# Performance work log

Measured on AMD Instinct MI355X. Metric: run time of the kernel, lower is better.

Reference implementation:

```python
import jax, jax.numpy as jnp
import numpy as np
from jax import lax

T = 64
TAU = 2.0
ALPHA = 4.0  # spikingjelly surrogate.Sigmoid default
V_TH = 1.0

@jax.custom_vjp
def spike(v):
    # Heaviside(v) with sigmoid surrogate gradient
    return (v >= 0.0).astype(v.dtype)

def _spike_fwd(v):
    return spike(v), v

def _spike_bwd(v, g):
    s = jax.nn.sigmoid(ALPHA * v)
    return (g * ALPHA * s * (1.0 - s),)

spike.defvjp(_spike_fwd, _spike_bwd)

def setup_inputs() -> dict:
    key = jax.random.key(0)
    k1, k2, k3 = jax.random.split(key, 3)
    x = jax.random.normal(k1, (2048, 28, 28), dtype=jnp.float32)
    W1 = jax.random.normal(k2, (1024, 784), dtype=jnp.float32) * (1.0 / np.sqrt(784))
    W2 = jax.random.normal(k3, (10, 1024), dtype=jnp.float32) * (1.0 / np.sqrt(1024))
    return {"x": x, "W1": W1, "W2": W2}

def _lif_step(v, c):
    # decay_input=True: v += (x - (v - v_reset)) / tau, v_reset = 0
    v = v + (c - v) / TAU
    s = spike(v - V_TH)
    v = v * (1.0 - s)  # hard reset to 0
    return v, s

def reference(x, W1, W2):
    B = x.shape[0]
    xf = x.reshape(B, -1)                      # [B, 784]
    c1 = xf @ W1.T                              # [B, 1024], identical every timestep
    v1_0 = jnp.zeros((B, W1.shape[0]), x.dtype)
    v2_0 = jnp.zeros((B, W2.shape[0]), x.dtype)

    def step(carry, _):
        v1, v2 = carry
        v1, s1 = _lif_step(v1, c1)              # [B, 1024]
        c2 = s1 @ W2.T                          # [B, 10]
        v2, s2 = _lif_step(v2, c2)              # [B, 10]
        return (v1, v2), s2

    _, out = lax.scan(step, (v1_0, v2_0), None, length=T)
    return out  # [T, B, 10]
```

## Files before the change

### kernel.cpp

```cpp
#include <hip/hip_runtime.h>
#include <stdint.h>

typedef unsigned long long u64;
typedef unsigned int u32;

#define T_STEPS 64
#define KDIM 784
#define N1 1024
#define NB 2048
#define N2 10

__global__ void k_w2t(const float* __restrict__ W2, float* __restrict__ W2T) {
    int j = blockIdx.x * blockDim.x + threadIdx.x;
    if (j >= N1) return;
    float r[12];
#pragma unroll
    for (int i = 0; i < 10; ++i) r[i] = W2[i * N1 + j];
    r[10] = 0.f; r[11] = 0.f;
#pragma unroll
    for (int i = 0; i < 12; ++i) W2T[j * 12 + i] = r[i];
}

__global__ __launch_bounds__(256) void k_transpose2(
    const float* __restrict__ X, float* __restrict__ Xt,
    const float* __restrict__ W1, float* __restrict__ W1t)
{
    __shared__ float t[32][33];
    int b = blockIdx.x;
    const float* src; float* dst; int R;
    int tile_r, tile_c;
    if (b < 1600) { src = X;  dst = Xt;  R = NB; tile_r = b / 25; tile_c = b % 25; }
    else { b -= 1600; src = W1; dst = W1t; R = N1; tile_r = b / 25; tile_c = b % 25; }

    const int tx = threadIdx.x & 31, ty = threadIdx.x >> 5;
    const int r0 = tile_r << 5, c0 = tile_c << 5;

#pragma unroll
    for (int i = 0; i < 32; i += 8) {
        int c = c0 + tx;
        t[ty + i][tx] = (c < KDIM) ? src[(size_t)(r0 + ty + i) * KDIM + c] : 0.f;
    }
    __syncthreads();
#pragma unroll
    for (int i = 0; i < 32; i += 8) {
        int c = c0 + ty + i;
        if (c < KDIM) dst[(size_t)c * R + r0 + tx] = t[tx][ty + i];
    }
}

#define NSTEP (KDIM / 16)

typedef const __attribute__((address_space(1))) void gas_void;
typedef __attribute__((address_space(3))) void las_void;

__global__ __launch_bounds__(256) void k_gemm_lif1(
    const float* __restrict__ Xt,
    const float* __restrict__ W1t,
    u64* __restrict__ bits)
{
    __shared__ __align__(16) float A2[4][16][64];
    __shared__ __align__(16) float B2[4][16][64];

    const int tid  = threadIdx.x;
    const int lane = tid & 63;
    const int tx   = tid & 15;
    const int ty   = tid >> 4;
    const int bm   = blockIdx.y << 6;
    const int bn   = blockIdx.x << 6;

    const int w4   = __builtin_amdgcn_readfirstlane((tid >> 6) << 2);
    const int srow = w4 + (lane >> 4);
    const int scol = (lane & 15) << 2;

    const float* gA = Xt  + (size_t)srow * NB + bm + scol;
    const float* gB = W1t + (size_t)srow * N1 + bn + scol;

#define STAGE(pp, t)                                                          \
    {                                                                         \
        __builtin_amdgcn_global_load_lds((gas_void*)(gA + (size_t)(t) * (16 * NB)), \
                                         (las_void*)&A2[pp][w4][0], 16, 0, 0); \
        __builtin_amdgcn_global_load_lds((gas_void*)(gB + (size_t)(t) * (16 * N1)), \
                                         (las_void*)&B2[pp][w4][0], 16, 0, 0); \
    }

#define COMPUTE(cur)                                                          \
    _Pragma("unroll")                                                         \
    for (int kk = 0; kk < 16; ++kk) {                                         \
        float4 av = *(const float4*)(&A2[cur][kk][ty << 2]);                  \
        float4 bv = *(const float4*)(&B2[cur][kk][tx << 2]);                  \
        acc[0][0] = fmaf(av.x, bv.x, acc[0][0]); acc[0][1] = fmaf(av.x, bv.y, acc[0][1]); \
        acc[0][2] = fmaf(av.x, bv.z, acc[0][2]); acc[0][3] = fmaf(av.x, bv.w, acc[0][3]); \
        acc[1][0] = fmaf(av.y, bv.x, acc[1][0]); acc[1][1] = fmaf(av.y, bv.y, acc[1][1]); \
        acc[1][2] = fmaf(av.y, bv.z, acc[1][2]); acc[1][3] = fmaf(av.y, bv.w, acc[1][3]); \
        acc[2][0] = fmaf(av.z, bv.x, acc[2][0]); acc[2][1] = fmaf(av.z, bv.y, acc[2][1]); \
        acc[2][2] = fmaf(av.z, bv.z, acc[2][2]); acc[2][3] = fmaf(av.z, bv.w, acc[2][3]); \
        acc[3][0] = fmaf(av.w, bv.x, acc[3][0]); acc[3][1] = fmaf(av.w, bv.y, acc[3][1]); \
        acc[3][2] = fmaf(av.w, bv.z, acc[3][2]); acc[3][3] = fmaf(av.w, bv.w, acc[3][3]); \
    }

    float acc[4][4];
#pragma unroll
    for (int r = 0; r < 4; ++r)
#pragma unroll
        for (int c = 0; c < 4; ++c) acc[r][c] = 0.f;

    STAGE(0, 0);
    STAGE(1, 1);

    for (int t = 0; t < NSTEP - 1; ++t) {
        asm volatile("s_waitcnt vmcnt(2)" ::: "memory");
        __builtin_amdgcn_sched_barrier(0);
        __builtin_amdgcn_s_barrier();
        __builtin_amdgcn_sched_barrier(0);
        if (t + 2 < NSTEP) STAGE((t + 2) & 3, t + 2);
        __builtin_amdgcn_sched_barrier(0);
        const int cur = t & 3;
        COMPUTE(cur);
        __builtin_amdgcn_sched_barrier(0);
    }
    asm volatile("s_waitcnt vmcnt(0)" ::: "memory");
    __builtin_amdgcn_sched_barrier(0);
    __builtin_amdgcn_s_barrier();
    __builtin_amdgcn_sched_barrier(0);
    {
        const int cur = (NSTEP - 1) & 3;
        COMPUTE(cur);
    }
#undef STAGE
#undef COMPUTE

    float c[16], v[16];
    u32 blo[16], bhi[16];
#pragma unroll
    for (int u = 0; u < 16; ++u) {
        c[u] = acc[u >> 2][u & 3];
        v[u] = 0.f; blo[u] = 0u; bhi[u] = 0u;
    }
    for (int t = 0; t < 32; ++t) {
#pragma unroll
        for (int u = 0; u < 16; ++u) {
            v[u] += (c[u] - v[u]) * 0.5f;
            bool s = v[u] >= 1.0f;
            blo[u] |= (s ? 1u : 0u) << t;
            v[u] = s ? 0.f : v[u];
        }
    }
    for (int t = 0; t < 32; ++t) {
#pragma unroll
        for (int u = 0; u < 16; ++u) {
            v[u] += (c[u] - v[u]) * 0.5f;
            bool s = v[u] >= 1.0f;
            bhi[u] |= (s ? 1u : 0u) << t;
            v[u] = s ? 0.f : v[u];
        }
    }
#pragma unroll
    for (int u = 0; u < 16; ++u) {
        int r = u >> 2, cc = u & 3;
        bits[(size_t)(bm + (ty << 2) + r) * N1 + (bn + (tx << 2) + cc)] =
            ((u64)bhi[u] << 32) | (u64)blo[u];
    }
}

__global__ __launch_bounds__(256) void k_c2(
    const u64* __restrict__ bits, const float* __restrict__ W2T,
    float* __restrict__ c2d)
{
    __shared__ u64  masksS[N1];
    __shared__ u32  idxS[N1];
    __shared__ float c2S[4][64][12];

    const int tid  = threadIdx.x;
    const int w    = tid >> 6;
    const int lane = tid & 63;
    const int b    = blockIdx.x;

    const u64* row = bits + (size_t)b * N1;
    const int base_j = w << 8;

    u64 mm[4];
#pragma unroll
    for (int q = 0; q < 4; ++q) mm[q] = row[base_j + (q << 6) + lane];

    int nact = 0;
#pragma unroll
    for (int q = 0; q < 4; ++q) {
        u64 ball = __ballot(mm[q] != 0ULL);
        int pos = nact + __popcll(ball & ((1ULL << lane) - 1ULL));
        if (mm[q] != 0ULL) { masksS[base_j + pos] = mm[q]; idxS[base_j + pos] = base_j + (q << 6) + lane; }
        nact += __popcll(ball);
    }
    const int npad = (nact + 3) & ~3;
    if (lane < npad - nact) { masksS[base_j + nact + lane] = 0ULL; idxS[base_j + nact + lane] = 0u; }

    float acc[10];
#pragma unroll
    for (int i = 0; i < 10; ++i) acc[i] = 0.f;

    for (int a = 0; a < npad; a += 4) {
        u64 m[4]; u32 j[4];
#pragma unroll
        for (int q = 0; q < 4; ++q) {
            m[q] = masksS[base_j + a + q];
            j[q] = idxS[base_j + a + q];
        }
#pragma unroll
        for (int q = 0; q < 4; ++q) {
            float sf = (float)((m[q] >> lane) & 1ULL);
            const float* wr = W2T + j[q] * 12;
            float4 w0 = *(const float4*)(wr);
            float4 w1 = *(const float4*)(wr + 4);
            float2 w2 = *(const float2*)(wr + 8);
            acc[0] = fmaf(sf, w0.x, acc[0]); acc[1] = fmaf(sf, w0.y, acc[1]);
            acc[2] = fmaf(sf, w0.z, acc[2]); acc[3] = fmaf(sf, w0.w, acc[3]);
            acc[4] = fmaf(sf, w1.x, acc[4]); acc[5] = fmaf(sf, w1.y, acc[5]);
            acc[6] = fmaf(sf, w1.z, acc[6]); acc[7] = fmaf(sf, w1.w, acc[7]);
            acc[8] = fmaf(sf, w2.x, acc[8]); acc[9] = fmaf(sf, w2.y, acc[9]);
        }
    }

#pragma unroll
    for (int i = 0; i < 10; ++i) c2S[w][lane][i] = acc[i];
    __syncthreads();

    for (int idx = tid; idx < 64 * 10; idx += 256) {
        int t = idx / 10, i = idx % 10;
        c2d[(size_t)b * 640 + idx] = ((c2S[0][t][i] + c2S[1][t][i]) + c2S[2][t][i]) + c2S[3][t][i];
    }
}

__global__ __launch_bounds__(256) void k_out(
    const float* __restrict__ c2d, float* __restrict__ out)
{
    const int p = blockIdx.x * 256 + threadIdx.x;
    const int b = p / 10, i = p % 10;
    const float* src = c2d + (size_t)b * 640 + i;

    float v2 = 0.f;
    for (int tb = 0; tb < 64; tb += 8) {
        float cc[8];
#pragma unroll
        for (int q = 0; q < 8; ++q) cc[q] = src[(tb + q) * 10];
#pragma unroll
        for (int q = 0; q < 8; ++q) {
            v2 += (cc[q] - v2) * 0.5f;
            bool s = v2 >= 1.0f;
            out[(size_t)(tb + q) * (NB * N2) + p] = s ? 1.f : 0.f;
            v2 = s ? 0.f : v2;
        }
    }
}

extern "C" void kernel_launch(void* const* d_in, const int* in_sizes, int n_in,
                              void* d_out, int out_size, void* d_ws, size_t ws_size,
                              hipStream_t stream) {
    const float* X  = (const float*)d_in[0];
    const float* W1 = (const float*)d_in[1];
    const float* W2 = (const float*)d_in[2];
    float* out = (float*)d_out;

    char* ws = (char*)d_ws;
    u64*   bits = (u64*)ws;
    float* W2T  = (float*)(ws + (size_t)NB * N1 * 8);
    float* Xt   = (float*)(ws + (size_t)NB * N1 * 8 + 65536);
    float* W1t  = Xt + (size_t)KDIM * NB;
    float* c2d  = W1t + (size_t)KDIM * N1;

    k_w2t<<<dim3((N1 + 255) / 256), dim3(256), 0, stream>>>(W2, W2T);
    k_transpose2<<<dim3(2400), dim3(256), 0, stream>>>(X, Xt, W1, W1t);

    dim3 g1(N1 / 64, NB / 64);
    k_gemm_lif1<<<g1, dim3(256), 0, stream>>>(Xt, W1t, bits);

    k_c2<<<dim3(NB), dim3(256), 0, stream>>>(bits, W2T, c2d);
    k_out<<<dim3(20480 / 256), dim3(256), 0, stream>>>(c2d, out);
}
```

Before: 180.1 us.

## Fuse prep kernels, register-prefetch GEMM, and fold output LIF into c2 kernel

```diff
diff --git a/kernel.cpp b/kernel.cpp
--- a/kernel.cpp
+++ b/kernel.cpp
@@ -10,23 +10,25 @@
 #define NB 2048
 #define N2 10
 
-__global__ void k_w2t(const float* __restrict__ W2, float* __restrict__ W2T) {
-    int j = blockIdx.x * blockDim.x + threadIdx.x;
-    if (j >= N1) return;
-    float r[12];
-#pragma unroll
-    for (int i = 0; i < 10; ++i) r[i] = W2[i * N1 + j];
-    r[10] = 0.f; r[11] = 0.f;
-#pragma unroll
-    for (int i = 0; i < 12; ++i) W2T[j * 12 + i] = r[i];
-}
-
-__global__ __launch_bounds__(256) void k_transpose2(
+__global__ __launch_bounds__(256) void k_prep(
     const float* __restrict__ X, float* __restrict__ Xt,
-    const float* __restrict__ W1, float* __restrict__ W1t)
+    const float* __restrict__ W1, float* __restrict__ W1t,
+    const float* __restrict__ W2, float* __restrict__ W2T)
 {
+    int b = blockIdx.x;
+    if (b == 2400) {
+        for (int it = 0; it < 4; ++it) {
+            int j = it * 256 + threadIdx.x;
+            float r[12];
+#pragma unroll
+            for (int i = 0; i < 10; ++i) r[i] = W2[i * N1 + j];
+            r[10] = 0.f; r[11] = 0.f;
+#pragma unroll
+            for (int i = 0; i < 12; ++i) W2T[j * 12 + i] = r[i];
+        }
+        return;
+    }
     __shared__ float t[32][33];
-    int b = blockIdx.x;
     const float* src; float* dst; int R;
     int tile_r, tile_c;
     if (b < 1600) { src = X;  dst = Xt;  R = NB; tile_r = b / 25; tile_c = b % 25; }
@@ -48,55 +50,28 @@
     }
 }
 
-#define NSTEP (KDIM / 16)
-
-typedef const __attribute__((address_space(1))) void gas_void;
-typedef __attribute__((address_space(3))) void las_void;
-
-__global__ __launch_bounds__(256) void k_gemm_lif1(
+__global__ __launch_bounds__(256, 2) void k_gemm_lif1(
     const float* __restrict__ Xt,
     const float* __restrict__ W1t,
     u64* __restrict__ bits)
 {
-    __shared__ __align__(16) float A2[4][16][64];
-    __shared__ __align__(16) float B2[4][16][64];
-
-    const int tid  = threadIdx.x;
-    const int lane = tid & 63;
-    const int tx   = tid & 15;
-    const int ty   = tid >> 4;
-    const int bm   = blockIdx.y << 6;
-    const int bn   = blockIdx.x << 6;
-
-    const int w4   = __builtin_amdgcn_readfirstlane((tid >> 6) << 2);
-    const int srow = w4 + (lane >> 4);
-    const int scol = (lane & 15) << 2;
-
-    const float* gA = Xt  + (size_t)srow * NB + bm + scol;
-    const float* gB = W1t + (size_t)srow * N1 + bn + scol;
-
-#define STAGE(pp, t)                                                          \
-    {                                                                         \
-        __builtin_amdgcn_global_load_lds((gas_void*)(gA + (size_t)(t) * (16 * NB)), \
-                                         (las_void*)&A2[pp][w4][0], 16, 0, 0); \
-        __builtin_amdgcn_global_load_lds((gas_void*)(gB + (size_t)(t) * (16 * N1)), \
-                                         (las_void*)&B2[pp][w4][0], 16, 0, 0); \
-    }
-
-#define COMPUTE(cur)                                                          \
-    _Pragma("unroll")                                                         \
-    for (int kk = 0; kk < 16; ++kk) {                                         \
-        float4 av = *(const float4*)(&A2[cur][kk][ty << 2]);                  \
-        float4 bv = *(const float4*)(&B2[cur][kk][tx << 2]);                  \
-        acc[0][0] = fmaf(av.x, bv.x, acc[0][0]); acc[0][1] = fmaf(av.x, bv.y, acc[0][1]); \
-        acc[0][2] = fmaf(av.x, bv.z, acc[0][2]); acc[0][3] = fmaf(av.x, bv.w, acc[0][3]); \
-        acc[1][0] = fmaf(av.y, bv.x, acc[1][0]); acc[1][1] = fmaf(av.y, bv.y, acc[1][1]); \
-        acc[1][2] = fmaf(av.y, bv.z, acc[1][2]); acc[1][3] = fmaf(av.y, bv.w, acc[1][3]); \
-        acc[2][0] = fmaf(av.z, bv.x, acc[2][0]); acc[2][1] = fmaf(av.z, bv.y, acc[2][1]); \
-        acc[2][2] = fmaf(av.z, bv.z, acc[2][2]); acc[2][3] = fmaf(av.z, bv.w, acc[2][3]); \
-        acc[3][0] = fmaf(av.w, bv.x, acc[3][0]); acc[3][1] = fmaf(av.w, bv.y, acc[3][1]); \
-        acc[3][2] = fmaf(av.w, bv.z, acc[3][2]); acc[3][3] = fmaf(av.w, bv.w, acc[3][3]); \
-    }
+    const int tid = threadIdx.x;
+    const int tx  = tid & 15;
+    const int ty  = tid >> 4;
+    const int bm  = blockIdx.y << 6;
+    const int bn  = blockIdx.x << 6;
+
+#define LOAD_A(k) (*(const float4*)(Xt  + (size_t)(k) * NB + bm + (ty << 2)))
+#define LOAD_B(k) (*(const float4*)(W1t + (size_t)(k) * N1 + bn + (tx << 2)))
+#define FMAS(av, bv)                                                                      \
+    acc[0][0] = fmaf(av.x, bv.x, acc[0][0]); acc[0][1] = fmaf(av.x, bv.y, acc[0][1]);     \
+    acc[0][2] = fmaf(av.x, bv.z, acc[0][2]); acc[0][3] = fmaf(av.x, bv.w, acc[0][3]);     \
+    acc[1][0] = fmaf(av.y, bv.x, acc[1][0]); acc[1][1] = fmaf(av.y, bv.y, acc[1][1]);     \
+    acc[1][2] = fmaf(av.y, bv.z, acc[1][2]); acc[1][3] = fmaf(av.y, bv.w, acc[1][3]);     \
+    acc[2][0] = fmaf(av.z, bv.x, acc[2][0]); acc[2][1] = fmaf(av.z, bv.y, acc[2][1]);     \
+    acc[2][2] = fmaf(av.z, bv.z, acc[2][2]); acc[2][3] = fmaf(av.z, bv.w, acc[2][3]);     \
+    acc[3][0] = fmaf(av.w, bv.x, acc[3][0]); acc[3][1] = fmaf(av.w, bv.y, acc[3][1]);     \
+    acc[3][2] = fmaf(av.w, bv.z, acc[3][2]); acc[3][3] = fmaf(av.w, bv.w, acc[3][3]);
 
     float acc[4][4];
 #pragma unroll
@@ -104,30 +79,27 @@
 #pragma unroll
         for (int c = 0; c < 4; ++c) acc[r][c] = 0.f;
 
-    STAGE(0, 0);
-    STAGE(1, 1);
-
-    for (int t = 0; t < NSTEP - 1; ++t) {
-        asm volatile("s_waitcnt vmcnt(2)" ::: "memory");
-        __builtin_amdgcn_sched_barrier(0);
-        __builtin_amdgcn_s_barrier();
-        __builtin_amdgcn_sched_barrier(0);
-        if (t + 2 < NSTEP) STAGE((t + 2) & 3, t + 2);
-        __builtin_amdgcn_sched_barrier(0);
-        const int cur = t & 3;
-        COMPUTE(cur);
-        __builtin_amdgcn_sched_barrier(0);
-    }
-    asm volatile("s_waitcnt vmcnt(0)" ::: "memory");
-    __builtin_amdgcn_sched_barrier(0);
-    __builtin_amdgcn_s_barrier();
-    __builtin_amdgcn_sched_barrier(0);
-    {
-        const int cur = (NSTEP - 1) & 3;
-        COMPUTE(cur);
-    }
-#undef STAGE
-#undef COMPUTE
+    float4 pa[16], pb[16];
+#pragma unroll
+    for (int q = 0; q < 16; ++q) { pa[q] = LOAD_A(q); pb[q] = LOAD_B(q); }
+
+    for (int t = 0; t < 48; ++t) {
+#pragma unroll
+        for (int q = 0; q < 16; ++q) {
+            float4 av = pa[q], bv = pb[q];
+            pa[q] = LOAD_A(t * 16 + 16 + q);
+            pb[q] = LOAD_B(t * 16 + 16 + q);
+            FMAS(av, bv);
+        }
+    }
+#pragma unroll
+    for (int q = 0; q < 16; ++q) {
+        float4 av = pa[q], bv = pb[q];
+        FMAS(av, bv);
+    }
+#undef LOAD_A
+#undef LOAD_B
+#undef FMAS
 
     float c[16], v[16];
     u32 blo[16], bhi[16];
@@ -162,13 +134,16 @@
     }
 }
 
-__global__ __launch_bounds__(256) void k_c2(
+__global__ __launch_bounds__(256) void k_c2lif(
     const u64* __restrict__ bits, const float* __restrict__ W2T,
-    float* __restrict__ c2d)
+    float* __restrict__ out)
 {
-    __shared__ u64  masksS[N1];
-    __shared__ u32  idxS[N1];
+    __shared__ u64   masksS[N1];
+    __shared__ u32   idxS[N1];
+    __shared__ float wS[4][64][12];
     __shared__ float c2S[4][64][12];
+    __shared__ float c2r[64][12];
+    __shared__ float s2S[64][10];
 
     const int tid  = threadIdx.x;
     const int w    = tid >> 6;
@@ -192,30 +167,42 @@
     }
     const int npad = (nact + 3) & ~3;
     if (lane < npad - nact) { masksS[base_j + nact + lane] = 0ULL; idxS[base_j + nact + lane] = 0u; }
+    asm volatile("s_waitcnt lgkmcnt(0)" ::: "memory");
 
     float acc[10];
 #pragma unroll
     for (int i = 0; i < 10; ++i) acc[i] = 0.f;
 
-    for (int a = 0; a < npad; a += 4) {
-        u64 m[4]; u32 j[4];
-#pragma unroll
-        for (int q = 0; q < 4; ++q) {
-            m[q] = masksS[base_j + a + q];
-            j[q] = idxS[base_j + a + q];
-        }
-#pragma unroll
-        for (int q = 0; q < 4; ++q) {
-            float sf = (float)((m[q] >> lane) & 1ULL);
-            const float* wr = W2T + j[q] * 12;
-            float4 w0 = *(const float4*)(wr);
-            float4 w1 = *(const float4*)(wr + 4);
-            float2 w2 = *(const float2*)(wr + 8);
-            acc[0] = fmaf(sf, w0.x, acc[0]); acc[1] = fmaf(sf, w0.y, acc[1]);
-            acc[2] = fmaf(sf, w0.z, acc[2]); acc[3] = fmaf(sf, w0.w, acc[3]);
-            acc[4] = fmaf(sf, w1.x, acc[4]); acc[5] = fmaf(sf, w1.y, acc[5]);
-            acc[6] = fmaf(sf, w1.z, acc[6]); acc[7] = fmaf(sf, w1.w, acc[7]);
-            acc[8] = fmaf(sf, w2.x, acc[8]); acc[9] = fmaf(sf, w2.y, acc[9]);
+    for (int base = 0; base < npad; base += 64) {
+        const int cnt = min(64, npad - base);
+        if (lane < cnt) {
+            int j = (int)idxS[base_j + base + lane];
+            const float4* src = (const float4*)(W2T + j * 12);
+            float4 a = src[0], bq = src[1], cq = src[2];
+            *(float4*)&wS[w][lane][0] = a;
+            *(float4*)&wS[w][lane][4] = bq;
+            *(float4*)&wS[w][lane][8] = cq;
+        }
+        asm volatile("s_waitcnt lgkmcnt(0) vmcnt(0)" ::: "memory");
+        __builtin_amdgcn_sched_barrier(0);
+
+        for (int a = 0; a < cnt; a += 4) {
+            u64 m[4];
+#pragma unroll
+            for (int q = 0; q < 4; ++q) m[q] = masksS[base_j + base + a + q];
+#pragma unroll
+            for (int q = 0; q < 4; ++q) {
+                float sf = (float)((m[q] >> lane) & 1ULL);
+                const float* wr = &wS[w][a + q][0];
+                float4 w0 = *(const float4*)(wr);
+                float4 w1 = *(const float4*)(wr + 4);
+                float2 w2 = *(const float2*)(wr + 8);
+                acc[0] = fmaf(sf, w0.x, acc[0]); acc[1] = fmaf(sf, w0.y, acc[1]);
+                acc[2] = fmaf(sf, w0.z, acc[2]); acc[3] = fmaf(sf, w0.w, acc[3]);
+                acc[4] = fmaf(sf, w1.x, acc[4]); acc[5] = fmaf(sf, w1.y, acc[5]);
+                acc[6] = fmaf(sf, w1.z, acc[6]); acc[7] = fmaf(sf, w1.w, acc[7]);
+                acc[8] = fmaf(sf, w2.x, acc[8]); acc[9] = fmaf(sf, w2.y, acc[9]);
+            }
         }
     }
 
@@ -225,29 +212,31 @@
 
     for (int idx = tid; idx < 64 * 10; idx += 256) {
         int t = idx / 10, i = idx % 10;
-        c2d[(size_t)b * 640 + idx] = ((c2S[0][t][i] + c2S[1][t][i]) + c2S[2][t][i]) + c2S[3][t][i];
-    }
-}
-
-__global__ __launch_bounds__(256) void k_out(
-    const float* __restrict__ c2d, float* __restrict__ out)
-{
-    const int p = blockIdx.x * 256 + threadIdx.x;
-    const int b = p / 10, i = p % 10;
-    const float* src = c2d + (size_t)b * 640 + i;
-
-    float v2 = 0.f;
-    for (int tb = 0; tb < 64; tb += 8) {
-        float cc[8];
-#pragma unroll
-        for (int q = 0; q < 8; ++q) cc[q] = src[(tb + q) * 10];
-#pragma unroll
-        for (int q = 0; q < 8; ++q) {
-            v2 += (cc[q] - v2) * 0.5f;
-            bool s = v2 >= 1.0f;
-            out[(size_t)(tb + q) * (NB * N2) + p] = s ? 1.f : 0.f;
-            v2 = s ? 0.f : v2;
-        }
+        c2r[t][i] = ((c2S[0][t][i] + c2S[1][t][i]) + c2S[2][t][i]) + c2S[3][t][i];
+    }
+    __syncthreads();
+
+    if (tid < 10) {
+        const int i = tid;
+        float v2 = 0.f;
+        for (int tb = 0; tb < 64; tb += 8) {
+            float cc[8];
+#pragma unroll
+            for (int q = 0; q < 8; ++q) cc[q] = c2r[tb + q][i];
+#pragma unroll
+            for (int q = 0; q < 8; ++q) {
+                v2 += (cc[q] - v2) * 0.5f;
+                bool s = v2 >= 1.0f;
+                s2S[tb + q][i] = s ? 1.f : 0.f;
+                v2 = s ? 0.f : v2;
+            }
+        }
+    }
+    __syncthreads();
+
+    for (int idx = tid; idx < 64 * 10; idx += 256) {
+        int t = idx / 10, i = idx % 10;
+        out[(size_t)t * (NB * N2) + (size_t)b * N2 + i] = s2S[t][i];
     }
 }
 
@@ -264,14 +253,11 @@
     float* W2T  = (float*)(ws + (size_t)NB * N1 * 8);
     float* Xt   = (float*)(ws + (size_t)NB * N1 * 8 + 65536);
     float* W1t  = Xt + (size_t)KDIM * NB;
-    float* c2d  = W1t + (size_t)KDIM * N1;
-
-    k_w2t<<<dim3((N1 + 255) / 256), dim3(256), 0, stream>>>(W2, W2T);
-    k_transpose2<<<dim3(2400), dim3(256), 0, stream>>>(X, Xt, W1, W1t);
+
+    k_prep<<<dim3(2401), dim3(256), 0, stream>>>(X, Xt, W1, W1t, W2, W2T);
 
     dim3 g1(N1 / 64, NB / 64);
     k_gemm_lif1<<<g1, dim3(256), 0, stream>>>(Xt, W1t, bits);
 
-    k_c2<<<dim3(NB), dim3(256), 0, stream>>>(bits, W2T, c2d);
-    k_out<<<dim3(20480 / 256), dim3(256), 0, stream>>>(c2d, out);
-}
+    k_c2lif<<<dim3(NB), dim3(256), 0, stream>>>(bits, W2T, out);
+}
```

After: 201.8 us. 12.1% more time.
